# Optimization experiments

Measured on AMD Instinct MI355X. Metric: run time of the kernel, lower is better.

Reference implementation:

```python
import jax, jax.numpy as jnp
import numpy as np

RC = 6.0            # cosine cutoff radius (Angstrom)
N_ANGULAR = 128     # module init arg; output dim = 3*N_ANGULAR
EPS = 1e-12


def cosine_cutoff(d):
    # Behler-style cosine cutoff: 0.5*(cos(pi*d/rc)+1) for d < rc, else 0
    return jnp.where(d < RC, 0.5 * (jnp.cos(jnp.pi * d / RC) + 1.0), 0.0)


def setup_inputs() -> dict:
    key = jax.random.key(0)
    k1, k2, k3, k4 = jax.random.split(key, 4)
    B, N, M = 8, 4096, 96
    L = 20.0  # box length
    positions = jax.random.uniform(k1, (B, N, 3), dtype=jnp.float32) * L
    cell = jnp.tile(jnp.eye(3, dtype=jnp.float32) * L, (B, 1, 1))
    neighbors = jax.random.randint(k2, (B, N, M), 0, N, dtype=jnp.int32)
    offsets = jax.random.randint(k3, (B, N, M, 3), -1, 2).astype(jnp.float32)
    mask = (jax.random.uniform(k4, (B, N, M)) > 0.1).astype(jnp.float32)
    return {"positions": positions, "cell": cell, "offsets": offsets,
            "mask": mask, "neighbors": neighbors}


def reference(positions, cell, offsets, mask, neighbors):
    B, N, M = neighbors.shape
    # gather neighbor positions: pos_j[b,n,m,:] = positions[b, neighbors[b,n,m], :]
    idx = neighbors.reshape(B, N * M)
    pos_j = jnp.take_along_axis(positions, idx[:, :, None], axis=1).reshape(B, N, M, 3)
    # displacement vectors with periodic offsets (offsets in cell coordinates)
    dis_vec = pos_j - positions[:, :, None, :] + jnp.einsum('bnmi,bij->bnmj', offsets, cell)
    distances = jnp.sqrt(jnp.sum(dis_vec * dis_vec, axis=-1) + EPS)  # [B,N,M]
    # cutoff / distance, zeroed where mask == 0
    cut = jnp.where(mask != 0.0, cosine_cutoff(distances) / distances, 0.0)
    # sort neighbors by descending cut value, gather cut-weighted vectors in that order
    order = jnp.argsort(-cut, axis=-1)                       # [B,N,M]
    cut_vec = cut[..., None] * dis_vec                       # [B,N,M,3]
    cut_vec = jnp.take_along_axis(cut_vec, order[..., None], axis=2)
    cut_vec = cut_vec.reshape(B, N, M * 3)
    # scatter into zero-padded descriptor of width 3*n_angular
    f = jnp.zeros((B, N, N_ANGULAR * 3), dtype=positions.dtype)
    f = f.at[:, :, : M * 3].set(cut_vec)
    return f
```

## Files before the change

kernel.cpp:

```cpp
#include <hip/hip_runtime.h>
#include <math.h>

#define M_NB  96
#define OUT_W 384
#define PPB   2

__global__ __launch_bounds__(PPB * M_NB) void deepmd_angular_kernel(
    const float* __restrict__ positions,
    const float* __restrict__ cell,
    const float* __restrict__ offsets,
    const float* __restrict__ mask,
    const int*   __restrict__ neighbors,
    float*       __restrict__ out,
    int N)
{
    __shared__ float cut_s[PPB][M_NB];
    __shared__ float out_s[PPB][3 * M_NB];

    const int m  = threadIdx.x;
    const int pr = threadIdx.y;
    const int p  = blockIdx.x * PPB + pr;
    const int b  = p / N;

    const long base_nm = (long)p * M_NB + m;
    const int   j   = neighbors[base_nm];
    const float msk = mask[base_nm];
    const float o0  = offsets[base_nm * 3 + 0];
    const float o1  = offsets[base_nm * 3 + 1];
    const float o2  = offsets[base_nm * 3 + 2];

    const float* cb = cell + (long)b * 9;
    const float c00 = cb[0], c01 = cb[1], c02 = cb[2];
    const float c10 = cb[3], c11 = cb[4], c12 = cb[5];
    const float c20 = cb[6], c21 = cb[7], c22 = cb[8];

    const float* pi_ = positions + (long)p * 3;
    const float* pj_ = positions + (long)(b * N + j) * 3;

    const float dx = pj_[0] - pi_[0] + o0 * c00 + o1 * c10 + o2 * c20;
    const float dy = pj_[1] - pi_[1] + o0 * c01 + o1 * c11 + o2 * c21;
    const float dz = pj_[2] - pi_[2] + o0 * c02 + o1 * c12 + o2 * c22;

    const float d = sqrtf(dx * dx + dy * dy + dz * dz + 1e-12f);

    float cut = 0.0f;
    if (msk != 0.0f && d < 6.0f) {
        cut = 0.5f * (cosf(d * 0.52359877559829887f) + 1.0f) / d;
    }

    cut_s[pr][m] = cut;
    out_s[pr][m]          = 0.0f;
    out_s[pr][m + M_NB]   = 0.0f;
    out_s[pr][m + 2*M_NB] = 0.0f;
    __syncthreads();

    if (cut != 0.0f) {
        int rank = 0;
        const float4* c4 = (const float4*)cut_s[pr];
        #pragma unroll
        for (int k4 = 0; k4 < M_NB / 4; ++k4) {
            const float4 c = c4[k4];
            const int k = 4 * k4;
            rank += (c.x > cut) || (c.x == cut && k + 0 < m);
            rank += (c.y > cut) || (c.y == cut && k + 1 < m);
            rank += (c.z > cut) || (c.z == cut && k + 2 < m);
            rank += (c.w > cut) || (c.w == cut && k + 3 < m);
        }
        out_s[pr][rank * 3 + 0] = cut * dx;
        out_s[pr][rank * 3 + 1] = cut * dy;
        out_s[pr][rank * 3 + 2] = cut * dz;
    }
    __syncthreads();

    float4 v;
    if (4 * m < 3 * M_NB) {
        v.x = out_s[pr][4 * m + 0];
        v.y = out_s[pr][4 * m + 1];
        v.z = out_s[pr][4 * m + 2];
        v.w = out_s[pr][4 * m + 3];
    } else {
        v.x = 0.0f; v.y = 0.0f; v.z = 0.0f; v.w = 0.0f;
    }
    ((float4*)(out + (size_t)p * OUT_W))[m] = v;
}

extern "C" void kernel_launch(void* const* d_in, const int* in_sizes, int n_in,
                              void* d_out, int out_size, void* d_ws, size_t ws_size,
                              hipStream_t stream) {
    const float* positions = (const float*)d_in[0];
    const float* cell      = (const float*)d_in[1];
    const float* offsets   = (const float*)d_in[2];
    const float* mask      = (const float*)d_in[3];
    const int*   neighbors = (const int*)d_in[4];
    float*       out       = (float*)d_out;

    const int BN = in_sizes[0] / 3;
    const int B  = in_sizes[1] / 9;
    const int N  = BN / B;

    dim3 block(M_NB, PPB, 1);
    dim3 grid(BN / PPB, 1, 1);
    deepmd_angular_kernel<<<grid, block, 0, stream>>>(
        positions, cell, offsets, mask, neighbors, out, N);
}
```

Baseline: 129.0 us.

## Map two points per wavefront with three neighbors per lane, dropping block barriers

Restructures the kernel so each 64-lane wavefront handles two points, with 32 lanes per point and three neighbors per lane. The cut-value exchange now stays inside the wavefront, so the two block-wide barriers go away and each lane has more independent loads in flight. The output row is zero-filled directly in global memory and each nonzero entry is then written straight to its sorted slot, replacing the shared-memory staging buffer and the coalesced float4 writeback. In exchange, the writes become scattered 4-byte stores that hit the same row twice. Correctness relies on lockstep execution within the wavefront and on the zero-fill stores landing before the scattered stores to the same addresses.

```diff
diff --git a/kernel.cpp b/kernel.cpp
--- a/kernel.cpp
+++ b/kernel.cpp
@@ -3,9 +3,9 @@
 
 #define M_NB  96
 #define OUT_W 384
-#define PPB   2
+#define PPBLK 8
 
-__global__ __launch_bounds__(PPB * M_NB) void deepmd_angular_kernel(
+__global__ __launch_bounds__(256) void deepmd_angular_kernel(
     const float* __restrict__ positions,
     const float* __restrict__ cell,
     const float* __restrict__ offsets,
@@ -14,74 +14,83 @@
     float*       __restrict__ out,
     int N)
 {
-    __shared__ float cut_s[PPB][M_NB];
-    __shared__ float out_s[PPB][3 * M_NB];
+    __shared__ float cut_s[4][2][M_NB];
 
-    const int m  = threadIdx.x;
-    const int pr = threadIdx.y;
-    const int p  = blockIdx.x * PPB + pr;
-    const int b  = p / N;
+    const int tid  = threadIdx.x;
+    const int wv   = tid >> 6;
+    const int lane = tid & 63;
+    const int h    = lane >> 5;
+    const int t    = lane & 31;
 
-    const long base_nm = (long)p * M_NB + m;
-    const int   j   = neighbors[base_nm];
-    const float msk = mask[base_nm];
-    const float o0  = offsets[base_nm * 3 + 0];
-    const float o1  = offsets[base_nm * 3 + 1];
-    const float o2  = offsets[base_nm * 3 + 2];
+    const int pblk = blockIdx.x * PPBLK;
+    const int b    = pblk / N;
+    const int p    = pblk + wv * 2 + h;
 
-    const float* cb = cell + (long)b * 9;
+    float4* orow = (float4*)(out + (size_t)(pblk + wv * 2) * OUT_W);
+    const float4 z4 = make_float4(0.f, 0.f, 0.f, 0.f);
+    orow[lane]       = z4;
+    orow[lane + 64]  = z4;
+    orow[lane + 128] = z4;
+
+    const float* cb = cell + (size_t)b * 9;
     const float c00 = cb[0], c01 = cb[1], c02 = cb[2];
     const float c10 = cb[3], c11 = cb[4], c12 = cb[5];
     const float c20 = cb[6], c21 = cb[7], c22 = cb[8];
 
-    const float* pi_ = positions + (long)p * 3;
-    const float* pj_ = positions + (long)(b * N + j) * 3;
+    const float pix = positions[(size_t)p * 3 + 0];
+    const float piy = positions[(size_t)p * 3 + 1];
+    const float piz = positions[(size_t)p * 3 + 2];
 
-    const float dx = pj_[0] - pi_[0] + o0 * c00 + o1 * c10 + o2 * c20;
-    const float dy = pj_[1] - pi_[1] + o0 * c01 + o1 * c11 + o2 * c21;
-    const float dz = pj_[2] - pi_[2] + o0 * c02 + o1 * c12 + o2 * c22;
-
-    const float d = sqrtf(dx * dx + dy * dy + dz * dz + 1e-12f);
-
-    float cut = 0.0f;
-    if (msk != 0.0f && d < 6.0f) {
-        cut = 0.5f * (cosf(d * 0.52359877559829887f) + 1.0f) / d;
+    int jn[3]; float mk[3], o0[3], o1[3], o2[3];
+    #pragma unroll
+    for (int i = 0; i < 3; ++i) {
+        const long e = (long)p * M_NB + t + 32 * i;
+        jn[i] = neighbors[e];
+        mk[i] = mask[e];
+        o0[i] = offsets[e * 3 + 0];
+        o1[i] = offsets[e * 3 + 1];
+        o2[i] = offsets[e * 3 + 2];
     }
 
-    cut_s[pr][m] = cut;
-    out_s[pr][m]          = 0.0f;
-    out_s[pr][m + M_NB]   = 0.0f;
-    out_s[pr][m + 2*M_NB] = 0.0f;
-    __syncthreads();
+    const long posb = (long)b * N * 3;
+    float dx[3], dy[3], dz[3], cut[3];
+    #pragma unroll
+    for (int i = 0; i < 3; ++i) {
+        const float* pj = positions + posb + (long)jn[i] * 3;
+        dx[i] = pj[0] - pix + o0[i] * c00 + o1[i] * c10 + o2[i] * c20;
+        dy[i] = pj[1] - piy + o0[i] * c01 + o1[i] * c11 + o2[i] * c21;
+        dz[i] = pj[2] - piz + o0[i] * c02 + o1[i] * c12 + o2[i] * c22;
+        const float d = sqrtf(dx[i] * dx[i] + dy[i] * dy[i] + dz[i] * dz[i] + 1e-12f);
+        float c = 0.f;
+        if (mk[i] != 0.f && d < 6.f)
+            c = 0.5f * (cosf(d * 0.52359877559829887f) + 1.f) / d;
+        cut[i] = c;
+        cut_s[wv][h][t + 32 * i] = c;
+    }
 
-    if (cut != 0.0f) {
-        int rank = 0;
-        const float4* c4 = (const float4*)cut_s[pr];
+    if (cut[0] != 0.f || cut[1] != 0.f || cut[2] != 0.f) {
+        __threadfence_block();
         #pragma unroll
-        for (int k4 = 0; k4 < M_NB / 4; ++k4) {
-            const float4 c = c4[k4];
-            const int k = 4 * k4;
-            rank += (c.x > cut) || (c.x == cut && k + 0 < m);
-            rank += (c.y > cut) || (c.y == cut && k + 1 < m);
-            rank += (c.z > cut) || (c.z == cut && k + 2 < m);
-            rank += (c.w > cut) || (c.w == cut && k + 3 < m);
+        for (int i = 0; i < 3; ++i) {
+            if (cut[i] == 0.f) continue;
+            const int m = t + 32 * i;
+            int rank = 0;
+            const float4* c4 = (const float4*)cut_s[wv][h];
+            #pragma unroll
+            for (int k4 = 0; k4 < M_NB / 4; ++k4) {
+                const float4 c = c4[k4];
+                const int k = 4 * k4;
+                rank += (c.x > cut[i]) || (c.x == cut[i] && k + 0 < m);
+                rank += (c.y > cut[i]) || (c.y == cut[i] && k + 1 < m);
+                rank += (c.z > cut[i]) || (c.z == cut[i] && k + 2 < m);
+                rank += (c.w > cut[i]) || (c.w == cut[i] && k + 3 < m);
+            }
+            float* dst = out + (size_t)p * OUT_W + rank * 3;
+            dst[0] = cut[i] * dx[i];
+            dst[1] = cut[i] * dy[i];
+            dst[2] = cut[i] * dz[i];
         }
-        out_s[pr][rank * 3 + 0] = cut * dx;
-        out_s[pr][rank * 3 + 1] = cut * dy;
-        out_s[pr][rank * 3 + 2] = cut * dz;
     }
-    __syncthreads();
-
-    float4 v;
-    if (4 * m < 3 * M_NB) {
-        v.x = out_s[pr][4 * m + 0];
-        v.y = out_s[pr][4 * m + 1];
-        v.z = out_s[pr][4 * m + 2];
-        v.w = out_s[pr][4 * m + 3];
-    } else {
-        v.x = 0.0f; v.y = 0.0f; v.z = 0.0f; v.w = 0.0f;
-    }
-    ((float4*)(out + (size_t)p * OUT_W))[m] = v;
 }
 
 extern "C" void kernel_launch(void* const* d_in, const int* in_sizes, int n_in,
@@ -98,8 +107,8 @@
     const int B  = in_sizes[1] / 9;
     const int N  = BN / B;
 
-    dim3 block(M_NB, PPB, 1);
-    dim3 grid(BN / PPB, 1, 1);
+    dim3 block(256, 1, 1);
+    dim3 grid(BN / PPBLK, 1, 1);
     deepmd_angular_kernel<<<grid, block, 0, stream>>>(
         positions, cell, offsets, mask, neighbors, out, N);
 }
```

Result: slower. 136.7 us (+6.0%).

## Split output zeroing into separate kernel and scatter results directly to global

Applied to the files above, without the earlier changes.

Replaces the shared-memory staging of the sorted output with a separate zero-fill kernel over the whole output, followed by a compute kernel that writes each neighbor's three values straight to global memory at its rank position. This removes the second barrier and the LDS staging buffer. In exchange, the output is written twice (once as zeros, then partly overwritten), there is an extra kernel launch, and the global stores become scattered 4-byte writes instead of coalesced float4 rows.

```diff
diff --git a/kernel.cpp b/kernel.cpp
--- a/kernel.cpp
+++ b/kernel.cpp
@@ -5,7 +5,17 @@
 #define OUT_W 384
 #define PPB   2
 
-__global__ __launch_bounds__(PPB * M_NB) void deepmd_angular_kernel(
+__global__ __launch_bounds__(256) void fill_zero_kernel(float4* __restrict__ out4,
+                                                        int total4)
+{
+    const int stride = gridDim.x * 256;
+    const float4 z4 = make_float4(0.f, 0.f, 0.f, 0.f);
+    #pragma unroll 4
+    for (int i = blockIdx.x * 256 + threadIdx.x; i < total4; i += stride)
+        out4[i] = z4;
+}
+
+__global__ __launch_bounds__(PPB * M_NB) void deepmd_angular_compute(
     const float* __restrict__ positions,
     const float* __restrict__ cell,
     const float* __restrict__ offsets,
@@ -15,7 +25,6 @@
     int N)
 {
     __shared__ float cut_s[PPB][M_NB];
-    __shared__ float out_s[PPB][3 * M_NB];
 
     const int m  = threadIdx.x;
     const int pr = threadIdx.y;
@@ -49,9 +58,6 @@
     }
 
     cut_s[pr][m] = cut;
-    out_s[pr][m]          = 0.0f;
-    out_s[pr][m + M_NB]   = 0.0f;
-    out_s[pr][m + 2*M_NB] = 0.0f;
     __syncthreads();
 
     if (cut != 0.0f) {
@@ -66,22 +72,11 @@
             rank += (c.z > cut) || (c.z == cut && k + 2 < m);
             rank += (c.w > cut) || (c.w == cut && k + 3 < m);
         }
-        out_s[pr][rank * 3 + 0] = cut * dx;
-        out_s[pr][rank * 3 + 1] = cut * dy;
-        out_s[pr][rank * 3 + 2] = cut * dz;
+        float* dst = out + (size_t)p * OUT_W + rank * 3;
+        dst[0] = cut * dx;
+        dst[1] = cut * dy;
+        dst[2] = cut * dz;
     }
-    __syncthreads();
-
-    float4 v;
-    if (4 * m < 3 * M_NB) {
-        v.x = out_s[pr][4 * m + 0];
-        v.y = out_s[pr][4 * m + 1];
-        v.z = out_s[pr][4 * m + 2];
-        v.w = out_s[pr][4 * m + 3];
-    } else {
-        v.x = 0.0f; v.y = 0.0f; v.z = 0.0f; v.w = 0.0f;
-    }
-    ((float4*)(out + (size_t)p * OUT_W))[m] = v;
 }
 
 extern "C" void kernel_launch(void* const* d_in, const int* in_sizes, int n_in,
@@ -98,8 +93,11 @@
     const int B  = in_sizes[1] / 9;
     const int N  = BN / B;
 
+    const int total4 = out_size / 4;
+    fill_zero_kernel<<<2048, 256, 0, stream>>>((float4*)out, total4);
+
     dim3 block(M_NB, PPB, 1);
     dim3 grid(BN / PPB, 1, 1);
-    deepmd_angular_kernel<<<grid, block, 0, stream>>>(
+    deepmd_angular_compute<<<grid, block, 0, stream>>>(
         positions, cell, offsets, mask, neighbors, out, N);
 }
```

New measurement: 139.1 us. +7.8%, slower.
